# Optimization experiments

Measured on AMD Instinct MI355X. Metric: run time of the kernel, lower is better.

## Reference

```python
import jax, jax.numpy as jnp
import numpy as np

B, N, DIN, DOUT, D, C = 64, 8192, 64, 64, 10, 4
NPC = N // C  # nodes per client


def setup_inputs() -> dict:
    key = jax.random.key(0)
    ks = jax.random.split(key, 6)
    x = jax.random.normal(ks[0], (B, N, DIN), dtype=jnp.float32)
    node_embeddings = jax.random.normal(ks[1], (N, D), dtype=jnp.float32)
    poly_coefficients = jax.random.normal(ks[2], (C, 1, 4), dtype=jnp.float32)  # unused in sprtrelu mode
    mask = jnp.ones((B, N, 1), dtype=jnp.float32)
    weights_pool = jax.random.normal(ks[3], (C, D, DIN, DOUT), dtype=jnp.float32)
    bias_pool = jax.random.normal(ks[4], (C, D, DOUT), dtype=jnp.float32)
    nodes_per = jnp.arange(N, dtype=jnp.int64 if jax.config.x64_enabled else jnp.int32).reshape(C, NPC)
    return {"x": x, "node_embeddings": node_embeddings, "poly_coefficients": poly_coefficients,
            "mask": mask, "weights_pool": weights_pool, "bias_pool": bias_pool, "nodes_per": nodes_per}


def reference(x, node_embeddings, poly_coefficients, mask, weights_pool, bias_pool, nodes_per):
    # active_mode='sprtrelu', inter_dropout=0.0 -> bernoulli mask is all ones,
    # so sum_EH is the sum of EH over ALL clients, identical for every client.
    c, n = nodes_per.shape
    b = x.shape[0]
    x = x * mask                                       # [B,N,Din]
    E = node_embeddings[nodes_per]                     # [C,n,D] client-wise gather
    xg = jnp.take(x, nodes_per.reshape(-1), axis=1).reshape(b, c, n, -1)  # [B,C,n,Din]
    tE = jax.nn.relu(E)                                # [C,n,D]
    # per-client EH_c = einsum('nd,bnc->bdc'); sum over clients (bernoulli all ones)
    sum_EH = jnp.einsum('cnd,bcni->bdi', tE, xg)       # [B,D,Din]
    # Z_c = H_c + transformed_E_c @ sum_EH
    Z = xg + jnp.einsum('cnd,bdi->bcni', tE, sum_EH)   # [B,C,n,Din]
    # dynamic per-node weights/bias from embeddings
    W = jnp.einsum('cnd,cdio->cnio', E, weights_pool)  # [C,n,Din,Dout]
    bb = jnp.einsum('cnd,cdo->cno', E, bias_pool)      # [C,n,Dout]
    out = jnp.einsum('bcni,cnio->bcno', Z, W) + bb     # [B,C,n,Dout]
    return out.reshape(b, c * n, -1)                   # concat over clients along node dim
```

## Files before the change

### kernel.cpp

```cpp
#include <hip/hip_runtime.h>
#include <hip/hip_bf16.h>


#define BB 64
#define NN 8192
#define DD 10
#define CC 4

typedef __bf16 bf16;
typedef __bf16 bf16x8 __attribute__((ext_vector_type(8)));
typedef float f32x4 __attribute__((ext_vector_type(4)));

__global__ __launch_bounds__(256, 4) void k_sumEH(
    const float* __restrict__ x, const float* __restrict__ emb,
    const float* __restrict__ mask, const int* __restrict__ np,
    float* __restrict__ sEH) {
  __shared__ int np_l[512];
  __shared__ float mask_l[512];
  __shared__ __align__(8) float tEm[512][DD];
  __shared__ __align__(16) float red[4][DD][64];

  const int b = blockIdx.x >> 4;
  const int chunk = blockIdx.x & 15;
  const int tid = threadIdx.x;
  const int lane = tid & 63;
  const int w = tid >> 6;

  for (int s = tid; s < 512; s += 256) {
    const int node = np[chunk * 512 + s];
    np_l[s] = node;
    mask_l[s] = mask[(size_t)b * NN + node];
  }
  __syncthreads();
  for (int s = tid; s < 2560; s += 256) {
    const int nl = s / 5, pr = s % 5;
    const float2 e = *(const float2*)(emb + (size_t)np_l[nl] * DD + pr * 2);
    const float m = mask_l[nl];
    tEm[nl][pr * 2] = fmaxf(e.x, 0.f) * m;
    tEm[nl][pr * 2 + 1] = fmaxf(e.y, 0.f) * m;
  }
  __syncthreads();

  const int qq = lane >> 4, r16 = lane & 15;
  const f32x4* x4 = (const f32x4*)(x + (size_t)b * NN * 64);
  f32x4 acc[DD];
#pragma unroll
  for (int d = 0; d < DD; ++d) acc[d] = (f32x4)0.f;

  const int wbase = w * 128;

  int idA[4], idB[4];
  f32x4 xvA[4], xvB[4];

#define LOAD_IDS(buf, s_)                                        \
  _Pragma("unroll") for (int t = 0; t < 4; ++t)                  \
      buf[t] = np_l[wbase + ((s_) * 4 + t) * 4 + qq];
#define LOAD_X(bufx, bufi)                                       \
  _Pragma("unroll") for (int t = 0; t < 4; ++t)                  \
      bufx[t] = x4[(size_t)bufi[t] * 16 + r16];
#define FMA_BATCH(bufx, s_)                                      \
  _Pragma("unroll") for (int t = 0; t < 4; ++t) {                \
    const int nl = wbase + ((s_) * 4 + t) * 4 + qq;              \
    const float2 t01 = *(const float2*)&tEm[nl][0];              \
    const float2 t23 = *(const float2*)&tEm[nl][2];              \
    const float2 t45 = *(const float2*)&tEm[nl][4];              \
    const float2 t67 = *(const float2*)&tEm[nl][6];              \
    const float2 t89 = *(const float2*)&tEm[nl][8];              \
    const f32x4 xv = bufx[t];                                    \
    acc[0] += xv * t01.x; acc[1] += xv * t01.y;                  \
    acc[2] += xv * t23.x; acc[3] += xv * t23.y;                  \
    acc[4] += xv * t45.x; acc[5] += xv * t45.y;                  \
    acc[6] += xv * t67.x; acc[7] += xv * t67.y;                  \
    acc[8] += xv * t89.x; acc[9] += xv * t89.y;                  \
  }

  LOAD_IDS(idA, 0)
  LOAD_X(xvA, idA)
#pragma unroll
  for (int ss = 0; ss < 4; ++ss) {
    LOAD_IDS(idB, 2 * ss + 1)
    LOAD_X(xvB, idB)
    FMA_BATCH(xvA, 2 * ss)
    if (ss < 3) {
      LOAD_IDS(idA, 2 * ss + 2)
      LOAD_X(xvA, idA)
    }
    FMA_BATCH(xvB, 2 * ss + 1)
  }
#undef LOAD_IDS
#undef LOAD_X
#undef FMA_BATCH

#pragma unroll
  for (int d = 0; d < DD; ++d) {
    f32x4 a = acc[d];
#pragma unroll
    for (int j = 0; j < 4; ++j) {
      float v = a[j];
      v += __shfl_xor(v, 16);
      v += __shfl_xor(v, 32);
      a[j] = v;
    }
    acc[d] = a;
  }
  if (qq == 0) {
#pragma unroll
    for (int d = 0; d < DD; ++d) *(f32x4*)&red[w][d][r16 * 4] = acc[d];
  }
  __syncthreads();

  for (int s = tid; s < DD * 64; s += 256) {
    const int d = s >> 6, i = s & 63;
    const float v = red[0][d][i] + red[1][d][i] + red[2][d][i] + red[3][d][i];
    atomicAdd(sEH + ((size_t)b * DD + d) * 64 + i, v);
  }
}

__global__ __launch_bounds__(512, 4) void k_main(
    const float* __restrict__ x, const float* __restrict__ emb,
    const float* __restrict__ mask, const float* __restrict__ wp,
    const float* __restrict__ bp, const int* __restrict__ np,
    const float* __restrict__ sEH, float* __restrict__ out) {
  __shared__ float E_l[8][DD];
  __shared__ float bb_l[8][64];
  __shared__ float mask_l[64][8];
  __shared__ __align__(16) bf16 Wt[8][64][72];

  const int tid = threadIdx.x;
  const int lane = tid & 63;
  const int w = tid >> 6;
  const int p0 = blockIdx.x * 8;
  const int c = p0 >> 11;

  {
    const int bq = tid >> 3, g = tid & 7;
    mask_l[bq][g] = mask[(size_t)bq * NN + np[p0 + g]];
  }
  if (tid < 80) {
    const int g = tid / 10, d = tid % 10;
    E_l[g][d] = emb[(size_t)np[p0 + g] * DD + d];
  }
  __syncthreads();

  {
    f32x4 aLo[8], aHi[8];
#pragma unroll
    for (int p = 0; p < 8; ++p) { aLo[p] = (f32x4)0.f; aHi[p] = (f32x4)0.f; }
#pragma unroll
    for (int d = 0; d < DD; ++d) {
      f32x4 eLo, eHi;
      eLo[0] = E_l[0][d]; eLo[1] = E_l[1][d]; eLo[2] = E_l[2][d]; eLo[3] = E_l[3][d];
      eHi[0] = E_l[4][d]; eHi[1] = E_l[5][d]; eHi[2] = E_l[6][d]; eHi[3] = E_l[7][d];
      const float* base = wp + ((size_t)(c * DD + d) * 64 + w * 8) * 64 + lane;
#pragma unroll
      for (int p = 0; p < 8; ++p) {
        const float v = base[(size_t)p * 64];
        aLo[p] += eLo * v;
        aHi[p] += eHi * v;
      }
    }
#pragma unroll
    for (int g = 0; g < 8; ++g) {
      bf16x8 v;
#pragma unroll
      for (int p = 0; p < 8; ++p) v[p] = (bf16)((g < 4) ? aLo[p][g] : aHi[p][g - 4]);
      *(bf16x8*)&Wt[g][lane][w * 8] = v;
    }
    float bacc = 0.f;
#pragma unroll
    for (int d = 0; d < DD; ++d)
      bacc = fmaf(E_l[w][d], bp[((size_t)(c * DD + d)) * 64 + lane], bacc);
    bb_l[w][lane] = bacc;
  }
  __syncthreads();

  const int mynode = np[p0 + w];
  const int q = lane >> 4, r16 = lane & 15;

  bf16x8 wfrag[4][2];
#pragma unroll
  for (int nt = 0; nt < 4; ++nt)
#pragma unroll
    for (int kt = 0; kt < 2; ++kt)
      wfrag[nt][kt] = *(const bf16x8*)&Wt[w][nt * 16 + r16][kt * 32 + q * 8];

  float biasv[4];
#pragma unroll
  for (int nt = 0; nt < 4; ++nt) biasv[nt] = bb_l[w][nt * 16 + r16];

  float tEr[DD];
#pragma unroll
  for (int d = 0; d < DD; ++d) tEr[d] = fmaxf(E_l[w][d], 0.f);

  const f32x4* x4 = (const f32x4*)x;
  const f32x4* s4 = (const f32x4*)sEH;

#pragma unroll
  for (int chunk = 0; chunk < 4; ++chunk) {
    const int b = chunk * 16 + r16;
    const float m = mask_l[b][w];
    const size_t xrow = ((size_t)b * NN + mynode) * 16;
    f32x4 z00 = x4[xrow + q * 2 + 0] * m;
    f32x4 z01 = x4[xrow + q * 2 + 1] * m;
    f32x4 z10 = x4[xrow + 8 + q * 2 + 0] * m;
    f32x4 z11 = x4[xrow + 8 + q * 2 + 1] * m;
    const f32x4* sb = s4 + (size_t)b * DD * 16 + q * 2;
#pragma unroll
    for (int d = 0; d < DD; ++d) {
      const f32x4 s0 = sb[d * 16 + 0];
      const f32x4 s1 = sb[d * 16 + 1];
      const f32x4 s2 = sb[d * 16 + 8];
      const f32x4 s3 = sb[d * 16 + 9];
      const float t = tEr[d];
      z00 += s0 * t;
      z01 += s1 * t;
      z10 += s2 * t;
      z11 += s3 * t;
    }
    bf16x8 a0, a1;
#pragma unroll
    for (int j = 0; j < 4; ++j) {
      a0[j] = (bf16)z00[j];
      a0[4 + j] = (bf16)z01[j];
      a1[j] = (bf16)z10[j];
      a1[4 + j] = (bf16)z11[j];
    }
    f32x4 acc[4];
#pragma unroll
    for (int nt = 0; nt < 4; ++nt) {
      acc[nt][0] = biasv[nt]; acc[nt][1] = biasv[nt];
      acc[nt][2] = biasv[nt]; acc[nt][3] = biasv[nt];
    }
#pragma unroll
    for (int nt = 0; nt < 4; ++nt) {
      acc[nt] = __builtin_amdgcn_mfma_f32_16x16x32_bf16(a0, wfrag[nt][0], acc[nt], 0, 0, 0);
      acc[nt] = __builtin_amdgcn_mfma_f32_16x16x32_bf16(a1, wfrag[nt][1], acc[nt], 0, 0, 0);
    }
    const size_t pg = (size_t)(p0 + w);
#pragma unroll
    for (int nt = 0; nt < 4; ++nt) {
#pragma unroll
      for (int r = 0; r < 4; ++r) {
        const int bg = chunk * 16 + q * 4 + r;
        out[((size_t)bg * NN + pg) * 64 + nt * 16 + r16] = acc[nt][r];
      }
    }
  }
}

extern "C" void kernel_launch(void* const* d_in, const int* in_sizes, int n_in,
                              void* d_out, int out_size, void* d_ws, size_t ws_size,
                              hipStream_t stream) {
  const float* x    = (const float*)d_in[0];
  const float* emb  = (const float*)d_in[1];
  const float* mask = (const float*)d_in[3];
  const float* wp   = (const float*)d_in[4];
  const float* bp   = (const float*)d_in[5];
  const int*   np   = (const int*)d_in[6];
  float* out = (float*)d_out;
  float* sEH = (float*)d_ws;

  hipMemsetAsync(sEH, 0, (size_t)BB * DD * 64 * sizeof(float), stream);
  k_sumEH<<<dim3(BB * 16), dim3(256), 0, stream>>>(x, emb, mask, np, sEH);
  k_main<<<dim3(NN / 8), dim3(512), 0, stream>>>(x, emb, mask, wp, bp, np, sEH, out);
}
```

Before: 426.8 us.

## Drop LDS staging in sumEH and halve nodes per block in main kernel

The sumEH kernel no longer stages node ids, mask and relu'd embeddings in shared memory. Each thread now gathers the index, mask and embedding row directly from global memory inside a simpler loop unrolled by two, which removes two barriers and the LDS setup phase but issues redundant embedding loads. The main kernel now processes 4 nodes per 256-thread block instead of 8 per 512, doubling the grid. As a result each weights_pool element loaded is reused for only 4 nodes, so global traffic for the weight build roughly doubles. Launch bounds are reduced on both kernels.

```diff
diff --git a/kernel.cpp b/kernel.cpp
--- a/kernel.cpp
+++ b/kernel.cpp
@@ -5,19 +5,15 @@
 #define BB 64
 #define NN 8192
 #define DD 10
-#define CC 4
 
 typedef __bf16 bf16;
 typedef __bf16 bf16x8 __attribute__((ext_vector_type(8)));
 typedef float f32x4 __attribute__((ext_vector_type(4)));
 
-__global__ __launch_bounds__(256, 4) void k_sumEH(
+__global__ __launch_bounds__(256, 2) void k_sumEH(
     const float* __restrict__ x, const float* __restrict__ emb,
     const float* __restrict__ mask, const int* __restrict__ np,
     float* __restrict__ sEH) {
-  __shared__ int np_l[512];
-  __shared__ float mask_l[512];
-  __shared__ __align__(8) float tEm[512][DD];
   __shared__ __align__(16) float red[4][DD][64];
 
   const int b = blockIdx.x >> 4;
@@ -25,71 +21,35 @@
   const int tid = threadIdx.x;
   const int lane = tid & 63;
   const int w = tid >> 6;
-
-  for (int s = tid; s < 512; s += 256) {
-    const int node = np[chunk * 512 + s];
-    np_l[s] = node;
-    mask_l[s] = mask[(size_t)b * NN + node];
-  }
-  __syncthreads();
-  for (int s = tid; s < 2560; s += 256) {
-    const int nl = s / 5, pr = s % 5;
-    const float2 e = *(const float2*)(emb + (size_t)np_l[nl] * DD + pr * 2);
-    const float m = mask_l[nl];
-    tEm[nl][pr * 2] = fmaxf(e.x, 0.f) * m;
-    tEm[nl][pr * 2 + 1] = fmaxf(e.y, 0.f) * m;
-  }
-  __syncthreads();
-
   const int qq = lane >> 4, r16 = lane & 15;
+
   const f32x4* x4 = (const f32x4*)(x + (size_t)b * NN * 64);
+  const float* mb = mask + (size_t)b * NN;
+  const int* npb = np + chunk * 512 + w * 128;
+
   f32x4 acc[DD];
 #pragma unroll
   for (int d = 0; d < DD; ++d) acc[d] = (f32x4)0.f;
 
-  const int wbase = w * 128;
-
-  int idA[4], idB[4];
-  f32x4 xvA[4], xvB[4];
-
-#define LOAD_IDS(buf, s_)                                        \
-  _Pragma("unroll") for (int t = 0; t < 4; ++t)                  \
-      buf[t] = np_l[wbase + ((s_) * 4 + t) * 4 + qq];
-#define LOAD_X(bufx, bufi)                                       \
-  _Pragma("unroll") for (int t = 0; t < 4; ++t)                  \
-      bufx[t] = x4[(size_t)bufi[t] * 16 + r16];
-#define FMA_BATCH(bufx, s_)                                      \
-  _Pragma("unroll") for (int t = 0; t < 4; ++t) {                \
-    const int nl = wbase + ((s_) * 4 + t) * 4 + qq;              \
-    const float2 t01 = *(const float2*)&tEm[nl][0];              \
-    const float2 t23 = *(const float2*)&tEm[nl][2];              \
-    const float2 t45 = *(const float2*)&tEm[nl][4];              \
-    const float2 t67 = *(const float2*)&tEm[nl][6];              \
-    const float2 t89 = *(const float2*)&tEm[nl][8];              \
-    const f32x4 xv = bufx[t];                                    \
-    acc[0] += xv * t01.x; acc[1] += xv * t01.y;                  \
-    acc[2] += xv * t23.x; acc[3] += xv * t23.y;                  \
-    acc[4] += xv * t45.x; acc[5] += xv * t45.y;                  \
-    acc[6] += xv * t67.x; acc[7] += xv * t67.y;                  \
-    acc[8] += xv * t89.x; acc[9] += xv * t89.y;                  \
-  }
-
-  LOAD_IDS(idA, 0)
-  LOAD_X(xvA, idA)
-#pragma unroll
-  for (int ss = 0; ss < 4; ++ss) {
-    LOAD_IDS(idB, 2 * ss + 1)
-    LOAD_X(xvB, idB)
-    FMA_BATCH(xvA, 2 * ss)
-    if (ss < 3) {
-      LOAD_IDS(idA, 2 * ss + 2)
-      LOAD_X(xvA, idA)
-    }
-    FMA_BATCH(xvB, 2 * ss + 1)
-  }
-#undef LOAD_IDS
-#undef LOAD_X
-#undef FMA_BATCH
+#pragma unroll 2
+  for (int g = 0; g < 32; ++g) {
+    const int idx = npb[g * 4 + qq];
+    f32x4 xv = x4[(size_t)idx * 16 + r16];
+    const float m = mb[idx];
+    const float2* e2 = (const float2*)(emb + (size_t)idx * DD);
+    const float2 e0 = e2[0], e1 = e2[1], e4 = e2[2], e6 = e2[3], e8 = e2[4];
+    xv *= m;
+    acc[0] += xv * fmaxf(e0.x, 0.f);
+    acc[1] += xv * fmaxf(e0.y, 0.f);
+    acc[2] += xv * fmaxf(e1.x, 0.f);
+    acc[3] += xv * fmaxf(e1.y, 0.f);
+    acc[4] += xv * fmaxf(e4.x, 0.f);
+    acc[5] += xv * fmaxf(e4.y, 0.f);
+    acc[6] += xv * fmaxf(e6.x, 0.f);
+    acc[7] += xv * fmaxf(e6.y, 0.f);
+    acc[8] += xv * fmaxf(e8.x, 0.f);
+    acc[9] += xv * fmaxf(e8.y, 0.f);
+  }
 
 #pragma unroll
   for (int d = 0; d < DD; ++d) {
@@ -116,55 +76,51 @@
   }
 }
 
-__global__ __launch_bounds__(512, 4) void k_main(
+__global__ __launch_bounds__(256, 2) void k_main(
     const float* __restrict__ x, const float* __restrict__ emb,
     const float* __restrict__ mask, const float* __restrict__ wp,
     const float* __restrict__ bp, const int* __restrict__ np,
     const float* __restrict__ sEH, float* __restrict__ out) {
-  __shared__ float E_l[8][DD];
-  __shared__ float bb_l[8][64];
-  __shared__ float mask_l[64][8];
-  __shared__ __align__(16) bf16 Wt[8][64][72];
+  __shared__ float E_l[4][DD];
+  __shared__ float bb_l[4][64];
+  __shared__ float mask_l[64][4];
+  __shared__ __align__(16) bf16 Wt[4][64][72];
 
   const int tid = threadIdx.x;
   const int lane = tid & 63;
   const int w = tid >> 6;
-  const int p0 = blockIdx.x * 8;
+  const int p0 = blockIdx.x * 4;
   const int c = p0 >> 11;
 
   {
-    const int bq = tid >> 3, g = tid & 7;
+    const int bq = tid >> 2, g = tid & 3;
     mask_l[bq][g] = mask[(size_t)bq * NN + np[p0 + g]];
   }
-  if (tid < 80) {
+  if (tid < 40) {
     const int g = tid / 10, d = tid % 10;
     E_l[g][d] = emb[(size_t)np[p0 + g] * DD + d];
   }
   __syncthreads();
 
   {
-    f32x4 aLo[8], aHi[8];
-#pragma unroll
-    for (int p = 0; p < 8; ++p) { aLo[p] = (f32x4)0.f; aHi[p] = (f32x4)0.f; }
+    f32x4 accW[16];
+#pragma unroll
+    for (int p = 0; p < 16; ++p) accW[p] = (f32x4)0.f;
 #pragma unroll
     for (int d = 0; d < DD; ++d) {
-      f32x4 eLo, eHi;
-      eLo[0] = E_l[0][d]; eLo[1] = E_l[1][d]; eLo[2] = E_l[2][d]; eLo[3] = E_l[3][d];
-      eHi[0] = E_l[4][d]; eHi[1] = E_l[5][d]; eHi[2] = E_l[6][d]; eHi[3] = E_l[7][d];
-      const float* base = wp + ((size_t)(c * DD + d) * 64 + w * 8) * 64 + lane;
-#pragma unroll
-      for (int p = 0; p < 8; ++p) {
-        const float v = base[(size_t)p * 64];
-        aLo[p] += eLo * v;
-        aHi[p] += eHi * v;
-      }
-    }
-#pragma unroll
-    for (int g = 0; g < 8; ++g) {
-      bf16x8 v;
-#pragma unroll
-      for (int p = 0; p < 8; ++p) v[p] = (bf16)((g < 4) ? aLo[p][g] : aHi[p][g - 4]);
-      *(bf16x8*)&Wt[g][lane][w * 8] = v;
+      f32x4 ev;
+      ev[0] = E_l[0][d]; ev[1] = E_l[1][d]; ev[2] = E_l[2][d]; ev[3] = E_l[3][d];
+      const float* base = wp + ((size_t)(c * DD + d) * 64 + w * 16) * 64 + lane;
+#pragma unroll
+      for (int p = 0; p < 16; ++p) accW[p] += ev * base[(size_t)p * 64];
+    }
+#pragma unroll
+    for (int g = 0; g < 4; ++g) {
+      bf16x8 v0, v1;
+#pragma unroll
+      for (int p = 0; p < 8; ++p) { v0[p] = (bf16)accW[p][g]; v1[p] = (bf16)accW[p + 8][g]; }
+      *(bf16x8*)&Wt[g][lane][w * 16] = v0;
+      *(bf16x8*)&Wt[g][lane][w * 16 + 8] = v1;
     }
     float bacc = 0.f;
 #pragma unroll
@@ -262,5 +218,5 @@
 
   hipMemsetAsync(sEH, 0, (size_t)BB * DD * 64 * sizeof(float), stream);
   k_sumEH<<<dim3(BB * 16), dim3(256), 0, stream>>>(x, emb, mask, np, sEH);
-  k_main<<<dim3(NN / 8), dim3(512), 0, stream>>>(x, emb, mask, wp, bp, np, sEH, out);
+  k_main<<<dim3(NN / 4), dim3(256), 0, stream>>>(x, emb, mask, wp, bp, np, sEH, out);
 }
```

Result: faster. 414.2 us (-3.0%).
